# Kernel tuning notes

Measured on AMD Instinct MI355X. Metric: run time of the kernel, lower is better.

## Reference

```python
import jax, jax.numpy as jnp
import numpy as np
from jax import lax

B, NCH, T = 256, 32, 2000
NTF, NSF, NSUB, TK = 4, 40, 20, 25
NCLS = 4
NTAN = NSUB * (NSUB + 1) // 2
REIG_EPS = 1e-4


def setup_inputs() -> dict:
    key = jax.random.key(0)
    ks = jax.random.split(key, 8)
    x = jax.random.normal(ks[0], (B, NCH, T), dtype=jnp.float32)
    conv1_w = jax.random.normal(ks[1], (NTF, 1, 1, TK), dtype=jnp.float32) * 0.2
    conv1_b = jnp.zeros((NTF,), dtype=jnp.float32)
    conv2_w = jax.random.normal(ks[2], (NSF, NTF, NCH, 1), dtype=jnp.float32) * 0.1
    conv2_b = jnp.zeros((NSF,), dtype=jnp.float32)
    # BiMap weight: semi-orthogonal (n_subspace x n_spatial_filters) via QR
    A = jax.random.normal(ks[3], (NSF, NSUB), dtype=jnp.float32)
    Q, _ = jnp.linalg.qr(A)
    W_bimap = Q.T  # (NSUB, NSF), rows orthonormal
    clf_w = jax.random.normal(ks[4], (NCLS, NTAN), dtype=jnp.float32) * 0.05
    clf_b = jnp.zeros((NCLS,), dtype=jnp.float32)
    return {"x": x, "conv1_w": conv1_w, "conv1_b": conv1_b,
            "conv2_w": conv2_w, "conv2_b": conv2_b,
            "W_bimap": W_bimap, "clf_w": clf_w, "clf_b": clf_b}


def _forward(x, conv1_w, conv1_b, conv2_w, conv2_b, W_bimap, clf_w, clf_b):
    dn = ('NCHW', 'OIHW', 'NCHW')
    h = x[:, None, :, :]  # (B,1,NCH,T)
    # temporal conv, 'same' with reflect padding along time
    pl = (TK - 1) // 2
    pr = TK - 1 - pl
    hp = jnp.pad(h, ((0, 0), (0, 0), (0, 0), (pl, pr)), mode='reflect')
    h1 = lax.conv_general_dilated(hp, conv1_w, (1, 1), 'VALID', dimension_numbers=dn)
    h1 = h1 + conv1_b[None, :, None, None]  # (B,NTF,NCH,T)
    # spatial conv collapses channel axis
    h2 = lax.conv_general_dilated(h1, conv2_w, (1, 1), 'VALID', dimension_numbers=dn)
    h2 = h2 + conv2_b[None, :, None, None]  # (B,NSF,1,T)
    h2 = h2.reshape(B, NSF, T)
    # covariance pooling over time (unbiased)
    hm = h2 - h2.mean(axis=-1, keepdims=True)
    C = jnp.einsum('bft,bgt->bfg', hm, hm) / (T - 1)  # (B,NSF,NSF)
    # BiMap: S = W C W^T  -> (B,NSUB,NSUB)
    S = jnp.einsum('if,bfg,jg->bij', W_bimap, C, W_bimap)
    # ReEig: clamp eigenvalues at threshold
    w, U = jnp.linalg.eigh(S)
    w = jnp.maximum(w, REIG_EPS)
    S = jnp.einsum('bik,bk,bjk->bij', U, w, U)
    # LogEig: matrix log, take scaled upper triangle, flatten
    w2, U2 = jnp.linalg.eigh(S)
    L = jnp.einsum('bik,bk,bjk->bij', U2, jnp.log(w2), U2)
    iu, ju = jnp.triu_indices(NSUB)
    scale = jnp.where(iu == ju, 1.0, jnp.sqrt(2.0)).astype(L.dtype)
    z = L[:, iu, ju] * scale[None, :]  # (B, NTAN)
    return z @ clf_w.T + clf_b


def reference(x, conv1_w, conv1_b, conv2_w, conv2_b, W_bimap, clf_w, clf_b):
    return _forward(x, conv1_w, conv1_b, conv2_w, conv2_b, W_bimap, clf_w, clf_b)
```

## Files before the change

kernel.cpp:

```cpp
#include <hip/hip_runtime.h>
#include <math.h>

#define B_    256
#define NCH   32
#define T_    2000
#define NTF   4
#define NSF   40
#define NSUB  20
#define TK    25
#define NCLS  4
#define NTAN  210
#define NPAIR 820
#define ACC_STRIDE 860
#define TILE_T 250
#define NTILE  8
#define PL     12

#define ACC_FLOATS (B_*ACC_STRIDE)
#define W2Q_OFF ACC_FLOATS
#define W1T_OFF (W2Q_OFF + NSF*NTF*NCH)
#define CB_OFF  (W1T_OFF + NTF*TK)

#define XS_TSTR 36
#define H2_STR  252
#define LDS_DW  10080

typedef float v2f __attribute__((ext_vector_type(2)));
typedef float v4f __attribute__((ext_vector_type(4)));

__device__ __forceinline__ v2f fma2(v2f a, v2f b, v2f c) {
#if __has_builtin(__builtin_elementwise_fma)
    return __builtin_elementwise_fma(a, b, c);
#else
    v2f r; r.x = fmaf(a.x, b.x, c.x); r.y = fmaf(a.y, b.y, c.y); return r;
#endif
}

__device__ __forceinline__ v4f fma4(v4f a, v4f b, v4f c) {
#if __has_builtin(__builtin_elementwise_fma)
    return __builtin_elementwise_fma(a, b, c);
#else
    v4f r;
    r.x = fmaf(a.x, b.x, c.x); r.y = fmaf(a.y, b.y, c.y);
    r.z = fmaf(a.z, b.z, c.z); r.w = fmaf(a.w, b.w, c.w);
    return r;
#endif
}

__device__ __forceinline__ int pack_ut(int f, int g) {
    return f*NSF - (f*(f-1))/2 + (g - f);
}

__global__ void prep_kernel(const float* __restrict__ conv1_w,
                            const float* __restrict__ conv1_b,
                            const float* __restrict__ conv2_w,
                            const float* __restrict__ conv2_b,
                            float* __restrict__ ws) {
    int tid = threadIdx.x;
    float* w2q = ws + W2Q_OFF;
    float* w1t = ws + W1T_OFF;
    float* cb  = ws + CB_OFF;
    for (int i = tid; i < NSF*NTF*NCH; i += 256) {
        int j  = i & 3;
        int q  = i >> 2;
        int s4 = q % 10;
        int cf = q / 10;
        int f  = cf & 3;
        int c  = cf >> 2;
        int s  = 4*s4 + j;
        w2q[i] = conv2_w[(s*NTF + f)*NCH + c];
    }
    for (int i = tid; i < NTF*TK; i += 256) {
        int f = i & 3;
        int k = i >> 2;
        w1t[i] = conv1_w[f*TK + k];
    }
    if (tid < NSF) {
        float s = conv2_b[tid];
        #pragma unroll
        for (int f = 0; f < NTF; ++f) {
            float a = 0.f;
            for (int c = 0; c < NCH; ++c) a += conv2_w[(tid*NTF + f)*NCH + c];
            s = fmaf(a, conv1_b[f], s);
        }
        cb[tid] = s;
    }
}

__global__ __launch_bounds__(256, 3)
void conv_gram_kernel(const float* __restrict__ x,
                      const float* __restrict__ wts,
                      float* __restrict__ acc)
{
    __shared__ float lds[LDS_DW];

    const int tid  = threadIdx.x;
    const int bid  = blockIdx.x;
    const int b    = bid >> 3;
    const int tile = bid & 7;
    const int t0   = tile * TILE_T;

    const float* xb = x + (size_t)b*NCH*T_;
    for (int li = tid; li < NCH*280; li += 256) {
        int c = li / 280;
        int i = li - c*280;
        int tg = t0 + i - PL;
        tg = (tg < 0) ? -tg : tg;
        tg = (tg >= T_) ? (2*T_ - 2 - tg) : tg;
        lds[i*XS_TSTR + c] = xb[c*T_ + tg];
    }
    __syncthreads();

    const float4* w1t = (const float4*)(wts + W1T_OFF);
    const float4* w2q = (const float4*)(wts + W2Q_OFF);
    const float4* cb4 = (const float4*)(wts + CB_OFF);

    v4f acc4[10];
    #pragma unroll
    for (int s4 = 0; s4 < 10; ++s4) {
        float4 t = cb4[s4];
        v4f a; a.x = t.x; a.y = t.y; a.z = t.z; a.w = t.w;
        acc4[s4] = a;
    }

    #pragma clang loop unroll(disable)
    for (int ch = 0; ch < 4; ++ch) {
        v2f h1[16];
        #pragma unroll
        for (int i = 0; i < 16; ++i) h1[i] = (v2f)0.f;

        #pragma clang loop unroll(disable)
        for (int k = 0; k < TK; ++k) {
            float4 wq = w1t[k];
            v2f w01; w01.x = wq.x; w01.y = wq.y;
            v2f w23; w23.x = wq.z; w23.y = wq.w;
            const float4* xr = (const float4*)&lds[(tid + k)*XS_TSTR + 8*ch];
            float4 xa = xr[0];
            float4 xb4 = xr[1];
            float xv[8] = {xa.x, xa.y, xa.z, xa.w, xb4.x, xb4.y, xb4.z, xb4.w};
            #pragma unroll
            for (int c = 0; c < 8; ++c) {
                v2f xc; xc.x = xv[c]; xc.y = xv[c];
                h1[2*c]   = fma2(xc, w01, h1[2*c]);
                h1[2*c+1] = fma2(xc, w23, h1[2*c+1]);
            }
        }

        const float4* wp = w2q + (ch*8)*(NTF*10);
        #pragma unroll
        for (int c = 0; c < 8; ++c) {
            float hf[4] = {h1[2*c].x, h1[2*c].y, h1[2*c+1].x, h1[2*c+1].y};
            #pragma unroll
            for (int f = 0; f < 4; ++f) {
                v4f hb; hb.x = hf[f]; hb.y = hf[f]; hb.z = hf[f]; hb.w = hf[f];
                #pragma unroll
                for (int s4 = 0; s4 < 10; ++s4) {
                    float4 w = wp[(c*4 + f)*10 + s4];
                    v4f wv; wv.x = w.x; wv.y = w.y; wv.z = w.z; wv.w = w.w;
                    acc4[s4] = fma4(hb, wv, acc4[s4]);
                }
            }
        }
    }
    __syncthreads();

    if (tid < H2_STR) {
        const bool valid = (tid < TILE_T);
        #pragma unroll
        for (int s4 = 0; s4 < 10; ++s4) {
            v4f a = acc4[s4];
            lds[(4*s4+0)*H2_STR + tid] = valid ? a.x : 0.f;
            lds[(4*s4+1)*H2_STR + tid] = valid ? a.y : 0.f;
            lds[(4*s4+2)*H2_STR + tid] = valid ? a.z : 0.f;
            lds[(4*s4+3)*H2_STR + tid] = valid ? a.w : 0.f;
        }
    }
    __syncthreads();

    float* accb = acc + b*ACC_STRIDE;

    if (tid < 55) {
        int bf = 0, rem = tid;
        while (rem >= 10 - bf) { rem -= 10 - bf; bf++; }
        int bg = bf + rem;

        const float4* rA[4];
        const float4* rB[4];
        #pragma unroll
        for (int a = 0; a < 4; ++a) {
            rA[a] = (const float4*)&lds[(4*bf + a)*H2_STR];
            rB[a] = (const float4*)&lds[(4*bg + a)*H2_STR];
        }
        v2f accL[16], accH[16];
        #pragma unroll
        for (int i = 0; i < 16; ++i) { accL[i] = (v2f)0.f; accH[i] = (v2f)0.f; }

        #pragma unroll 7
        for (int q = 0; q < H2_STR/4; ++q) {
            float4 av[4], bv[4];
            #pragma unroll
            for (int a = 0; a < 4; ++a) av[a] = rA[a][q];
            #pragma unroll
            for (int a = 0; a < 4; ++a) bv[a] = rB[a][q];
            #pragma unroll
            for (int a = 0; a < 4; ++a) {
                v2f aL; aL.x = av[a].x; aL.y = av[a].y;
                v2f aH; aH.x = av[a].z; aH.y = av[a].w;
                #pragma unroll
                for (int g = 0; g < 4; ++g) {
                    v2f bL; bL.x = bv[g].x; bL.y = bv[g].y;
                    v2f bH; bH.x = bv[g].z; bH.y = bv[g].w;
                    accL[a*4+g] = fma2(aL, bL, accL[a*4+g]);
                    accH[a*4+g] = fma2(aH, bH, accH[a*4+g]);
                }
            }
        }
        #pragma unroll
        for (int a = 0; a < 4; ++a) {
            #pragma unroll
            for (int g = 0; g < 4; ++g) {
                int f  = 4*bf + a;
                int gg = 4*bg + g;
                if (f <= gg) {
                    v2f sL = accL[a*4+g], sH = accH[a*4+g];
                    float s = (sL.x + sL.y) + (sH.x + sH.y);
                    atomicAdd(&accb[pack_ut(f, gg)], s);
                }
            }
        }
    }

    if (tid >= 64 && tid < 64 + NSF) {
        int row = tid - 64;
        const float4* rr = (const float4*)&lds[row*H2_STR];
        float csum = 0.f;
        #pragma unroll 7
        for (int q = 0; q < H2_STR/4; ++q) {
            float4 v = rr[q];
            csum += (v.x + v.y) + (v.z + v.w);
        }
        atomicAdd(&accb[NPAIR + row], csum);
    }
}

__device__ __forceinline__ void pq_sched(int r, int k, int& p, int& q) {
    if (k == 0) { p = 19; q = r; }
    else {
        int a = r + k;      if (a >= 19) a -= 19;
        int d = r - k + 19; if (d >= 19) d -= 19;
        p = a; q = d;
    }
}

__global__ __launch_bounds__(128)
void finalize_kernel(const float* __restrict__ acc,
                     const float* __restrict__ W_bimap,
                     const float* __restrict__ clf_w,
                     const float* __restrict__ clf_b,
                     float* __restrict__ out)
{
    __shared__ float C[NSF*NSF];
    __shared__ float Wb[NSUB*NSF];
    __shared__ float M[NSUB*NSF];
    __shared__ float A[NSUB*21];
    __shared__ float V[NSUB*21];
    __shared__ float cs_c[10], cs_s[10];
    __shared__ float lam[NSUB];
    __shared__ float z[NTAN];

    const int tid = threadIdx.x;
    const int b   = blockIdx.x;
    const float* accb = acc + b*ACC_STRIDE;

    for (int i = tid; i < NSF*NSF; i += 128) {
        int f = i / NSF, g = i % NSF;
        int lo = f < g ? f : g;
        int hi = f < g ? g : f;
        double G  = (double)accb[pack_ut(lo, hi)];
        double sf = (double)accb[NPAIR + f];
        double sg = (double)accb[NPAIR + g];
        C[i] = (float)((G - sf*sg/(double)T_) / (double)(T_ - 1));
    }
    for (int i = tid; i < NSUB*NSF; i += 128) Wb[i] = W_bimap[i];
    __syncthreads();

    for (int i = tid; i < NSUB*NSF; i += 128) {
        int r = i / NSF, g = i % NSF;
        float s = 0.f;
        #pragma unroll 8
        for (int f = 0; f < NSF; ++f) s = fmaf(Wb[r*NSF+f], C[f*NSF+g], s);
        M[i] = s;
    }
    __syncthreads();

    for (int i = tid; i < NSUB*NSUB; i += 128) {
        int r = i / NSUB, j = i % NSUB;
        float s = 0.f;
        #pragma unroll 8
        for (int g = 0; g < NSF; ++g) s = fmaf(M[r*NSF+g], Wb[j*NSF+g], s);
        A[r*21+j] = s;
        V[r*21+j] = (r == j) ? 1.f : 0.f;
    }
    __syncthreads();

    const int kk = tid / 10;
    const int ll = tid - 10*(tid/10);

    for (int sweep = 0; sweep < 7; ++sweep) {
        for (int r = 0; r < 19; ++r) {
            if (tid < 10) {
                int p, q; pq_sched(r, tid, p, q);
                float app = A[p*21+p], aqq = A[q*21+q], apq = A[p*21+q];
                float c = 1.f, s = 0.f;
                if (fabsf(apq) > 1e-30f) {
                    float tau = (aqq - app) / (2.f*apq);
                    float t = 1.f / (fabsf(tau) + sqrtf(1.f + tau*tau));
                    if (tau < 0.f) t = -t;
                    c = 1.f / sqrtf(1.f + t*t);
                    s = t * c;
                }
                cs_c[tid] = c; cs_s[tid] = s;
            }
            __syncthreads();
            if (tid < 100) {
                int pk, qk, pl, ql;
                pq_sched(r, kk, pk, qk);
                pq_sched(r, ll, pl, ql);
                float ck = cs_c[kk], sk = cs_s[kk];
                float cl = cs_c[ll], sl = cs_s[ll];
                float a00 = A[pk*21+pl], a01 = A[pk*21+ql];
                float a10 = A[qk*21+pl], a11 = A[qk*21+ql];
                float t00 = ck*a00 - sk*a10, t01 = ck*a01 - sk*a11;
                float t10 = sk*a00 + ck*a10, t11 = sk*a01 + ck*a11;
                A[pk*21+pl] = cl*t00 - sl*t01;
                A[pk*21+ql] = sl*t00 + cl*t01;
                A[qk*21+pl] = cl*t10 - sl*t11;
                A[qk*21+ql] = sl*t10 + cl*t11;
                float v00 = V[pk*21+pl], v01 = V[pk*21+ql];
                float v10 = V[qk*21+pl], v11 = V[qk*21+ql];
                V[pk*21+pl] = cl*v00 - sl*v01;
                V[pk*21+ql] = sl*v00 + cl*v01;
                V[qk*21+pl] = cl*v10 - sl*v11;
                V[qk*21+ql] = sl*v10 + cl*v11;
            }
            __syncthreads();
        }
    }

    if (tid < NSUB) {
        float w = A[tid*21+tid];
        lam[tid] = logf(fmaxf(w, 1e-4f));
    }
    __syncthreads();

    for (int p = tid; p < NTAN; p += 128) {
        int i = 0, rem = p;
        while (rem >= NSUB - i) { rem -= NSUB - i; i++; }
        int j = i + rem;
        float s = 0.f;
        #pragma unroll 5
        for (int k = 0; k < NSUB; ++k) s = fmaf(V[i*21+k]*lam[k], V[j*21+k], s);
        z[p] = (i == j) ? s : s * 1.41421356237309515f;
    }
    __syncthreads();

    if (tid < NCLS) {
        float s = clf_b[tid];
        for (int p = 0; p < NTAN; ++p) s = fmaf(clf_w[tid*NTAN+p], z[p], s);
        out[b*NCLS + tid] = s;
    }
}

extern "C" void kernel_launch(void* const* d_in, const int* in_sizes, int n_in,
                              void* d_out, int out_size, void* d_ws, size_t ws_size,
                              hipStream_t stream) {
    const float* x       = (const float*)d_in[0];
    const float* conv1_w = (const float*)d_in[1];
    const float* conv1_b = (const float*)d_in[2];
    const float* conv2_w = (const float*)d_in[3];
    const float* conv2_b = (const float*)d_in[4];
    const float* W_bimap = (const float*)d_in[5];
    const float* clf_w   = (const float*)d_in[6];
    const float* clf_b   = (const float*)d_in[7];
    float* out = (float*)d_out;
    float* ws  = (float*)d_ws;

    hipMemsetAsync(ws, 0, (size_t)ACC_FLOATS*sizeof(float), stream);

    prep_kernel<<<1, 256, 0, stream>>>(conv1_w, conv1_b, conv2_w, conv2_b, ws);
    conv_gram_kernel<<<B_*NTILE, 256, 0, stream>>>(x, ws, ws);
    finalize_kernel<<<B_, 128, 0, stream>>>(ws, W_bimap, clf_w, clf_b, out);
}
```

Baseline: 336.2 us.

## Split Gram accumulation across four time chunks, fold row sums, shrink finalize block

The Gram stage in conv_gram_kernel now uses 220 threads rather than 55. Each group of 55 threads covers a quarter of the time tile, so per-thread serial work drops about 4x, at the cost of 4x more atomicAdds to the accumulator. The separate row-sum pass is removed; diagonal block threads now accumulate the column sums during the Gram loop. The finalize kernel shrinks to 64 threads, a single wavefront, with each thread doing up to two Jacobi rotation updates, which should make its barriers cheaper.

Result: slower. 602.5 us (+79.2%).

```diff
diff --git a/kernel.cpp b/kernel.cpp
--- a/kernel.cpp
+++ b/kernel.cpp
@@ -179,10 +179,15 @@
 
     float* accb = acc + b*ACC_STRIDE;
 
-    if (tid < 55) {
-        int bf = 0, rem = tid;
+    if (tid < 220) {
+        const int qc = tid / 55;
+        const int u  = tid - 55*qc;
+        int bf = 0, rem = u;
         while (rem >= 10 - bf) { rem -= 10 - bf; bf++; }
-        int bg = bf + rem;
+        const int bg = bf + rem;
+        const bool diag = (bf == bg);
+        const int qs = qc * 16;
+        const int qe = (qc == 3) ? 63 : qs + 16;
 
         const float4* rA[4];
         const float4* rB[4];
@@ -194,14 +199,24 @@
         v2f accL[16], accH[16];
         #pragma unroll
         for (int i = 0; i < 16; ++i) { accL[i] = (v2f)0.f; accH[i] = (v2f)0.f; }
-
-        #pragma unroll 7
-        for (int q = 0; q < H2_STR/4; ++q) {
+        v4f cs4[4];
+        #pragma unroll
+        for (int a = 0; a < 4; ++a) cs4[a] = (v4f)0.f;
+
+        #pragma unroll 4
+        for (int q = qs; q < qe; ++q) {
             float4 av[4], bv[4];
             #pragma unroll
             for (int a = 0; a < 4; ++a) av[a] = rA[a][q];
             #pragma unroll
             for (int a = 0; a < 4; ++a) bv[a] = rB[a][q];
+            if (diag) {
+                #pragma unroll
+                for (int a = 0; a < 4; ++a) {
+                    v4f t; t.x = av[a].x; t.y = av[a].y; t.z = av[a].z; t.w = av[a].w;
+                    cs4[a] += t;
+                }
+            }
             #pragma unroll
             for (int a = 0; a < 4; ++a) {
                 v2f aL; aL.x = av[a].x; aL.y = av[a].y;
@@ -228,18 +243,14 @@
                 }
             }
         }
-    }
-
-    if (tid >= 64 && tid < 64 + NSF) {
-        int row = tid - 64;
-        const float4* rr = (const float4*)&lds[row*H2_STR];
-        float csum = 0.f;
-        #pragma unroll 7
-        for (int q = 0; q < H2_STR/4; ++q) {
-            float4 v = rr[q];
-            csum += (v.x + v.y) + (v.z + v.w);
-        }
-        atomicAdd(&accb[NPAIR + row], csum);
+        if (diag) {
+            #pragma unroll
+            for (int a = 0; a < 4; ++a) {
+                v4f t = cs4[a];
+                float s = (t.x + t.y) + (t.z + t.w);
+                atomicAdd(&accb[NPAIR + 4*bf + a], s);
+            }
+        }
     }
 }
 
@@ -252,7 +263,33 @@
     }
 }
 
-__global__ __launch_bounds__(128)
+__device__ __forceinline__ void jacobi_update(float* A, float* V,
+                                              const float* cs_c, const float* cs_s,
+                                              int r, int item) {
+    int kk = item / 10;
+    int ll = item - 10*kk;
+    int pk, qk, pl, ql;
+    pq_sched(r, kk, pk, qk);
+    pq_sched(r, ll, pl, ql);
+    float ck = cs_c[kk], sk = cs_s[kk];
+    float cl = cs_c[ll], sl = cs_s[ll];
+    float a00 = A[pk*21+pl], a01 = A[pk*21+ql];
+    float a10 = A[qk*21+pl], a11 = A[qk*21+ql];
+    float t00 = ck*a00 - sk*a10, t01 = ck*a01 - sk*a11;
+    float t10 = sk*a00 + ck*a10, t11 = sk*a01 + ck*a11;
+    A[pk*21+pl] = cl*t00 - sl*t01;
+    A[pk*21+ql] = sl*t00 + cl*t01;
+    A[qk*21+pl] = cl*t10 - sl*t11;
+    A[qk*21+ql] = sl*t10 + cl*t11;
+    float v00 = V[pk*21+pl], v01 = V[pk*21+ql];
+    float v10 = V[qk*21+pl], v11 = V[qk*21+ql];
+    V[pk*21+pl] = cl*v00 - sl*v01;
+    V[pk*21+ql] = sl*v00 + cl*v01;
+    V[qk*21+pl] = cl*v10 - sl*v11;
+    V[qk*21+ql] = sl*v10 + cl*v11;
+}
+
+__global__ __launch_bounds__(64)
 void finalize_kernel(const float* __restrict__ acc,
                      const float* __restrict__ W_bimap,
                      const float* __restrict__ clf_w,
@@ -272,7 +309,7 @@
     const int b   = blockIdx.x;
     const float* accb = acc + b*ACC_STRIDE;
 
-    for (int i = tid; i < NSF*NSF; i += 128) {
+    for (int i = tid; i < NSF*NSF; i += 64) {
         int f = i / NSF, g = i % NSF;
         int lo = f < g ? f : g;
         int hi = f < g ? g : f;
@@ -281,10 +318,10 @@
         double sg = (double)accb[NPAIR + g];
         C[i] = (float)((G - sf*sg/(double)T_) / (double)(T_ - 1));
     }
-    for (int i = tid; i < NSUB*NSF; i += 128) Wb[i] = W_bimap[i];
-    __syncthreads();
-
-    for (int i = tid; i < NSUB*NSF; i += 128) {
+    for (int i = tid; i < NSUB*NSF; i += 64) Wb[i] = W_bimap[i];
+    __syncthreads();
+
+    for (int i = tid; i < NSUB*NSF; i += 64) {
         int r = i / NSF, g = i % NSF;
         float s = 0.f;
         #pragma unroll 8
@@ -293,7 +330,7 @@
     }
     __syncthreads();
 
-    for (int i = tid; i < NSUB*NSUB; i += 128) {
+    for (int i = tid; i < NSUB*NSUB; i += 64) {
         int r = i / NSUB, j = i % NSUB;
         float s = 0.f;
         #pragma unroll 8
@@ -302,9 +339,6 @@
         V[r*21+j] = (r == j) ? 1.f : 0.f;
     }
     __syncthreads();
-
-    const int kk = tid / 10;
-    const int ll = tid - 10*(tid/10);
 
     for (int sweep = 0; sweep < 7; ++sweep) {
         for (int r = 0; r < 19; ++r) {
@@ -322,27 +356,8 @@
                 cs_c[tid] = c; cs_s[tid] = s;
             }
             __syncthreads();
-            if (tid < 100) {
-                int pk, qk, pl, ql;
-                pq_sched(r, kk, pk, qk);
-                pq_sched(r, ll, pl, ql);
-                float ck = cs_c[kk], sk = cs_s[kk];
-                float cl = cs_c[ll], sl = cs_s[ll];
-                float a00 = A[pk*21+pl], a01 = A[pk*21+ql];
-                float a10 = A[qk*21+pl], a11 = A[qk*21+ql];
-                float t00 = ck*a00 - sk*a10, t01 = ck*a01 - sk*a11;
-                float t10 = sk*a00 + ck*a10, t11 = sk*a01 + ck*a11;
-                A[pk*21+pl] = cl*t00 - sl*t01;
-                A[pk*21+ql] = sl*t00 + cl*t01;
-                A[qk*21+pl] = cl*t10 - sl*t11;
-                A[qk*21+ql] = sl*t10 + cl*t11;
-                float v00 = V[pk*21+pl], v01 = V[pk*21+ql];
-                float v10 = V[qk*21+pl], v11 = V[qk*21+ql];
-                V[pk*21+pl] = cl*v00 - sl*v01;
-                V[pk*21+ql] = sl*v00 + cl*v01;
-                V[qk*21+pl] = cl*v10 - sl*v11;
-                V[qk*21+ql] = sl*v10 + cl*v11;
-            }
+            jacobi_update(A, V, cs_c, cs_s, r, tid);
+            if (tid < 36) jacobi_update(A, V, cs_c, cs_s, r, tid + 64);
             __syncthreads();
         }
     }
@@ -353,7 +368,7 @@
     }
     __syncthreads();
 
-    for (int p = tid; p < NTAN; p += 128) {
+    for (int p = tid; p < NTAN; p += 64) {
         int i = 0, rem = p;
         while (rem >= NSUB - i) { rem -= NSUB - i; i++; }
         int j = i + rem;
@@ -389,5 +404,5 @@
 
     prep_kernel<<<1, 256, 0, stream>>>(conv1_w, conv1_b, conv2_w, conv2_b, ws);
     conv_gram_kernel<<<B_*NTILE, 256, 0, stream>>>(x, ws, ws);
-    finalize_kernel<<<B_, 128, 0, stream>>>(ws, W_bimap, clf_w, clf_b, out);
-}
+    finalize_kernel<<<B_, 64, 0, stream>>>(ws, W_bimap, clf_w, clf_b, out);
+}
```

## Swizzle h2 LDS layout, raise occupancy, fold memset into prep kernel

Applied to the files above, without the earlier changes.

Pads the h2 LDS rows to 256 floats and XOR-swizzles the float4 columns by row group, so the Gram-matrix readers hit different banks instead of conflicting. Launch bounds go from 3 to 4 blocks per CU to allow more resident waves. The separate hipMemsetAsync is removed; the accumulator is now zeroed by a 256-block prep kernel, cutting one launch. Risks are higher register pressure under the tighter bounds and wrong reads at chunks 63 and above if the swizzle misses any index.

Result: no change. 337.4 us (+0.4%).

```diff
diff --git a/kernel.cpp b/kernel.cpp
--- a/kernel.cpp
+++ b/kernel.cpp
@@ -22,8 +22,9 @@
 #define CB_OFF  (W1T_OFF + NTF*TK)
 
 #define XS_TSTR 36
-#define H2_STR  252
-#define LDS_DW  10080
+#define H2_STR  256
+#define H2_CHK  63
+#define LDS_DW  10240
 
 typedef float v2f __attribute__((ext_vector_type(2)));
 typedef float v4f __attribute__((ext_vector_type(4)));
@@ -57,6 +58,9 @@
                             const float* __restrict__ conv2_b,
                             float* __restrict__ ws) {
     int tid = threadIdx.x;
+    for (int i = blockIdx.x*256 + tid; i < ACC_FLOATS; i += 256*256) ws[i] = 0.f;
+    if (blockIdx.x != 0) return;
+
     float* w2q = ws + W2Q_OFF;
     float* w1t = ws + W1T_OFF;
     float* cb  = ws + CB_OFF;
@@ -87,7 +91,7 @@
     }
 }
 
-__global__ __launch_bounds__(256, 3)
+__global__ __launch_bounds__(256, 4)
 void conv_gram_kernel(const float* __restrict__ x,
                       const float* __restrict__ wts,
                       float* __restrict__ acc)
@@ -164,15 +168,18 @@
     }
     __syncthreads();
 
-    if (tid < H2_STR) {
+    if (tid < 252) {
         const bool valid = (tid < TILE_T);
+        const int qw = tid >> 2;
+        const int ew = tid & 3;
         #pragma unroll
         for (int s4 = 0; s4 < 10; ++s4) {
             v4f a = acc4[s4];
-            lds[(4*s4+0)*H2_STR + tid] = valid ? a.x : 0.f;
-            lds[(4*s4+1)*H2_STR + tid] = valid ? a.y : 0.f;
-            lds[(4*s4+2)*H2_STR + tid] = valid ? a.z : 0.f;
-            lds[(4*s4+3)*H2_STR + tid] = valid ? a.w : 0.f;
+            const int col = (((qw ^ (s4 & 7)) << 2) | ew);
+            lds[(4*s4+0)*H2_STR + col] = valid ? a.x : 0.f;
+            lds[(4*s4+1)*H2_STR + col] = valid ? a.y : 0.f;
+            lds[(4*s4+2)*H2_STR + col] = valid ? a.z : 0.f;
+            lds[(4*s4+3)*H2_STR + col] = valid ? a.w : 0.f;
         }
     }
     __syncthreads();
@@ -183,6 +190,8 @@
         int bf = 0, rem = tid;
         while (rem >= 10 - bf) { rem -= 10 - bf; bf++; }
         int bg = bf + rem;
+        const int xa = bf & 7;
+        const int xbq = bg & 7;
 
         const float4* rA[4];
         const float4* rB[4];
@@ -196,12 +205,12 @@
         for (int i = 0; i < 16; ++i) { accL[i] = (v2f)0.f; accH[i] = (v2f)0.f; }
 
         #pragma unroll 7
-        for (int q = 0; q < H2_STR/4; ++q) {
+        for (int q = 0; q < H2_CHK; ++q) {
             float4 av[4], bv[4];
             #pragma unroll
-            for (int a = 0; a < 4; ++a) av[a] = rA[a][q];
-            #pragma unroll
-            for (int a = 0; a < 4; ++a) bv[a] = rB[a][q];
+            for (int a = 0; a < 4; ++a) av[a] = rA[a][q ^ xa];
+            #pragma unroll
+            for (int a = 0; a < 4; ++a) bv[a] = rB[a][q ^ xbq];
             #pragma unroll
             for (int a = 0; a < 4; ++a) {
                 v2f aL; aL.x = av[a].x; aL.y = av[a].y;
@@ -232,11 +241,12 @@
 
     if (tid >= 64 && tid < 64 + NSF) {
         int row = tid - 64;
+        const int xr = (row >> 2) & 7;
         const float4* rr = (const float4*)&lds[row*H2_STR];
         float csum = 0.f;
         #pragma unroll 7
-        for (int q = 0; q < H2_STR/4; ++q) {
-            float4 v = rr[q];
+        for (int q = 0; q < H2_CHK; ++q) {
+            float4 v = rr[q ^ xr];
             csum += (v.x + v.y) + (v.z + v.w);
         }
         atomicAdd(&accb[NPAIR + row], csum);
@@ -385,9 +395,7 @@
     float* out = (float*)d_out;
     float* ws  = (float*)d_ws;
 
-    hipMemsetAsync(ws, 0, (size_t)ACC_FLOATS*sizeof(float), stream);
-
-    prep_kernel<<<1, 256, 0, stream>>>(conv1_w, conv1_b, conv2_w, conv2_b, ws);
+    prep_kernel<<<256, 256, 0, stream>>>(conv1_w, conv1_b, conv2_w, conv2_b, ws);
     conv_gram_kernel<<<B_*NTILE, 256, 0, stream>>>(x, ws, ws);
     finalize_kernel<<<B_, 128, 0, stream>>>(ws, W_bimap, clf_w, clf_b, out);
 }
```
